# Kernel optimization log

Measured on AMD Instinct MI355X. Metric: run time of the kernel, lower is better.

The kernel has to match this reference:

```python
import jax, jax.numpy as jnp
import numpy as np
import math

B, S, D = 8, 1024, 1024
H, R = 16, 8
HD = D // H
SCALING = 16.0 / R  # alpha / rank = 2.0
DFF = 4 * D
DC = D // 2
NC = 3


def setup_inputs() -> dict:
    key = jax.random.key(0)
    ks = jax.random.split(key, 32)
    n = lambda i, shape, s=0.02: jax.random.normal(ks[i], shape, dtype=jnp.float32) * s
    inp = {
        'hidden_states': jax.random.normal(ks[0], (B, S, D), dtype=jnp.float32),
        # LoRA-adapted projections: base weight W [out,in], lora_A [r,in], lora_B [out,r]
        'Wq': n(1, (D, D)), 'Aq': n(2, (R, D), 0.1), 'Bq': n(3, (D, R), 0.02),
        'Wk': n(4, (D, D)), 'Ak': n(5, (R, D), 0.1), 'Bk': n(6, (D, R), 0.02),
        'Wv': n(7, (D, D)), 'Av': n(8, (R, D), 0.1), 'Bv': n(9, (D, R), 0.02),
        'Wo': n(10, (D, D)), 'Ao': n(11, (R, D), 0.1), 'Bo': n(12, (D, R), 0.02),
        'ln1_g': jnp.ones((D,), jnp.float32), 'ln1_b': jnp.zeros((D,), jnp.float32),
        'ln2_g': jnp.ones((D,), jnp.float32), 'ln2_b': jnp.zeros((D,), jnp.float32),
        'W1': n(13, (DFF, D)), 'b1': jnp.zeros((DFF,), jnp.float32),
        'W2': n(14, (D, DFF)), 'b2': jnp.zeros((D,), jnp.float32),
        'Wc1': n(15, (DC, D)), 'bc1': jnp.zeros((DC,), jnp.float32),
        'Wc2': n(16, (NC, DC)), 'bc2': jnp.zeros((NC,), jnp.float32),
    }
    return inp


def _lora_linear(x, W, A, Bm):
    # F.linear(x, W) + scaling * F.linear(F.linear(x, A), B)
    return x @ W.T + SCALING * ((x @ A.T) @ Bm.T)


def _layer_norm(x, g, b, eps=1e-5):
    mu = jnp.mean(x, axis=-1, keepdims=True)
    var = jnp.var(x, axis=-1, keepdims=True)
    return (x - mu) * jax.lax.rsqrt(var + eps) * g + b


def reference(hidden_states, Wq, Aq, Bq, Wk, Ak, Bk, Wv, Av, Bv, Wo, Ao, Bo,
              ln1_g, ln1_b, ln2_g, ln2_b, W1, b1, W2, b2, Wc1, bc1, Wc2, bc2):
    residual = hidden_states
    h = _layer_norm(hidden_states, ln1_g, ln1_b)
    # attention
    q = _lora_linear(h, Wq, Aq, Bq).reshape(B, S, H, HD).transpose(0, 2, 1, 3)
    k = _lora_linear(h, Wk, Ak, Bk).reshape(B, S, H, HD).transpose(0, 2, 1, 3)
    v = _lora_linear(h, Wv, Av, Bv).reshape(B, S, H, HD).transpose(0, 2, 1, 3)
    scores = jnp.einsum('bhqd,bhkd->bhqk', q, k) / math.sqrt(HD)
    probs = jax.nn.softmax(scores, axis=-1)
    ctx = jnp.einsum('bhqk,bhkd->bhqd', probs, v)
    ctx = ctx.transpose(0, 2, 1, 3).reshape(B, S, D)
    attn_out = _lora_linear(ctx, Wo, Ao, Bo)
    h = residual + attn_out
    residual = h
    hn = _layer_norm(h, ln2_g, ln2_b)
    ffn = jax.nn.gelu(hn @ W1.T + b1, approximate=False) @ W2.T + b2
    h = residual + ffn
    pooled = h[:, 0]  # [B, D]
    logits = jax.nn.gelu(pooled @ Wc1.T + bc1, approximate=False) @ Wc2.T + bc2
    return logits
```

## Files before the change

### kernel.cpp

```cpp
#include <hip/hip_runtime.h>
#include <hip/hip_bf16.h>


typedef __bf16 bf16x8 __attribute__((ext_vector_type(8)));
typedef float f32x4 __attribute__((ext_vector_type(4)));

__device__ __forceinline__ float bf2f(unsigned short u) {
  union { unsigned int i; float f; } v; v.i = ((unsigned int)u) << 16; return v.f;
}
__device__ __forceinline__ unsigned short f2bf(float f) {
  union { float f; unsigned int i; } v; v.f = f;
  unsigned int u = v.i;
  u += 0x7FFFu + ((u >> 16) & 1u);
  return (unsigned short)(u >> 16);
}
__device__ __forceinline__ float gelu_exact(float x) {
  return 0.5f * x * (1.0f + erff(x * 0.70710678118654752440f));
}

__global__ __launch_bounds__(256) void fold_kernel(
    const float* __restrict__ W, const float* __restrict__ A,
    const float* __restrict__ Bm, void* __restrict__ out, int out_bf16) {
  int i = blockIdx.x * 256 + threadIdx.x;
  int n = i >> 10, k = i & 1023;
  float acc = W[i];
#pragma unroll
  for (int r = 0; r < 8; ++r) acc += 2.0f * Bm[n * 8 + r] * A[r * 1024 + k];
  if (out_bf16) ((unsigned short*)out)[i] = f2bf(acc);
  else          ((float*)out)[i] = acc;
}

__global__ __launch_bounds__(256) void ln_kernel(
    const float* __restrict__ x, long in_stride, const float* __restrict__ g,
    const float* __restrict__ b, void* __restrict__ out, int out_bf16) {
  const float* xr = x + (size_t)blockIdx.x * in_stride;
  int t = threadIdx.x;
  float4 v = ((const float4*)xr)[t];
  float s  = v.x + v.y + v.z + v.w;
  float sq = v.x * v.x + v.y * v.y + v.z * v.z + v.w * v.w;
#pragma unroll
  for (int o = 32; o; o >>= 1) { s += __shfl_down(s, o); sq += __shfl_down(sq, o); }
  __shared__ float rs_[4], rq_[4], stat[2];
  int w = t >> 6, l = t & 63;
  if (l == 0) { rs_[w] = s; rq_[w] = sq; }
  __syncthreads();
  if (t == 0) {
    float S = rs_[0] + rs_[1] + rs_[2] + rs_[3];
    float Q = rq_[0] + rq_[1] + rq_[2] + rq_[3];
    float mu = S * (1.0f / 1024.0f);
    float var = Q * (1.0f / 1024.0f) - mu * mu;
    stat[0] = mu; stat[1] = rsqrtf(var + 1e-5f);
  }
  __syncthreads();
  float mu = stat[0], rstd = stat[1];
  float4 gg = ((const float4*)g)[t];
  float4 bb = ((const float4*)b)[t];
  float o0 = (v.x - mu) * rstd * gg.x + bb.x;
  float o1 = (v.y - mu) * rstd * gg.y + bb.y;
  float o2 = (v.z - mu) * rstd * gg.z + bb.z;
  float o3 = (v.w - mu) * rstd * gg.w + bb.w;
  if (out_bf16) {
    unsigned short* op = (unsigned short*)out + (size_t)blockIdx.x * 1024 + t * 4;
    op[0] = f2bf(o0); op[1] = f2bf(o1); op[2] = f2bf(o2); op[3] = f2bf(o3);
  } else {
    float* op = (float*)out + (size_t)blockIdx.x * 1024 + t * 4;
    op[0] = o0; op[1] = o1; op[2] = o2; op[3] = o3;
  }
}

__device__ __forceinline__ void gload_lds16(const void* g, void* l) {
  __builtin_amdgcn_global_load_lds(
      (__attribute__((address_space(1))) void*)(g),
      (__attribute__((address_space(3))) void*)(l), 16, 0, 0);
}

__global__ __launch_bounds__(256, 2) void gemm_kv(
    const unsigned short* __restrict__ h,
    const unsigned short* __restrict__ Wk, const unsigned short* __restrict__ Wv,
    unsigned short* __restrict__ Kout, unsigned short* __restrict__ Vout) {
  __shared__ unsigned short sA[128 * 32];
  __shared__ unsigned short sB[128 * 32];
  int wg = blockIdx.x;
  int swz = (wg & 7) * 128 + (wg >> 3);
  int proj = swz >> 9;
  int rem = swz & 511;
  int nb = rem & 7, mb = rem >> 3;
  const unsigned short* W = proj ? Wv : Wk;
  unsigned short* C = proj ? Vout : Kout;
  int brow = mb << 7, bcol = nb << 7;
  int t = threadIdx.x;
  int w = t >> 6, l = t & 63;
  int wr = (w >> 1) << 6, wc = (w & 1) << 6;
  int frow = l & 15, fk = (l >> 4) << 3;
  f32x4 acc[4][4];
#pragma unroll
  for (int m = 0; m < 4; ++m)
#pragma unroll
    for (int n = 0; n < 4; ++n) acc[m][n] = (f32x4){0.f, 0.f, 0.f, 0.f};
  int e0 = (w * 2) * 512 + l * 8;
  int e1 = e0 + 512;
  int r0 = e0 >> 5, c0 = e0 & 31;
  int r1 = e1 >> 5, c1 = e1 & 31;
  const unsigned short* gA0 = h + (size_t)(brow + r0) * 1024 + c0;
  const unsigned short* gA1 = h + (size_t)(brow + r1) * 1024 + c1;
  const unsigned short* gB0 = W + (size_t)(bcol + r0) * 1024 + c0;
  const unsigned short* gB1 = W + (size_t)(bcol + r1) * 1024 + c1;
  for (int kt = 0; kt < 1024; kt += 32) {
    gload_lds16(gA0 + kt, &sA[e0]);
    gload_lds16(gA1 + kt, &sA[e1]);
    gload_lds16(gB0 + kt, &sB[e0]);
    gload_lds16(gB1 + kt, &sB[e1]);
    __syncthreads();
    bf16x8 a[4], b[4];
#pragma unroll
    for (int m = 0; m < 4; ++m)
      a[m] = *(const bf16x8*)&sA[(wr + m * 16 + frow) * 32 + fk];
#pragma unroll
    for (int n = 0; n < 4; ++n)
      b[n] = *(const bf16x8*)&sB[(wc + n * 16 + frow) * 32 + fk];
#pragma unroll
    for (int m = 0; m < 4; ++m)
#pragma unroll
      for (int n = 0; n < 4; ++n)
        acc[m][n] = __builtin_amdgcn_mfma_f32_16x16x32_bf16(a[m], b[n], acc[m][n], 0, 0, 0);
    __syncthreads();
  }
  int crow = (l >> 4) << 2, ccol = l & 15;
#pragma unroll
  for (int m = 0; m < 4; ++m) {
    int gr = brow + wr + m * 16 + crow;
#pragma unroll
    for (int n = 0; n < 4; ++n) {
      int gc = bcol + wc + n * 16 + ccol;
#pragma unroll
      for (int j = 0; j < 4; ++j)
        C[(size_t)(gr + j) * 1024 + gc] = f2bf(acc[m][n][j]);
    }
  }
}

template <int CPW>
__global__ __launch_bounds__(256) void skinny_gemm(
    const float* __restrict__ X,
    const float* __restrict__ W,
    const float* __restrict__ bias,
    const float* __restrict__ resid, long rstride,
    float* __restrict__ Y, int N, int K, int do_gelu) {
  __shared__ float sX[8][1024];
  int t = threadIdx.x, w = t >> 6, l = t & 63;
  int col0 = blockIdx.x * (4 * CPW) + w * CPW;
  float acc[CPW][8];
#pragma unroll
  for (int c = 0; c < CPW; ++c)
#pragma unroll
    for (int m = 0; m < 8; ++m) acc[c][m] = 0.f;
  for (int kc = 0; kc < K; kc += 1024) {
    for (int i = t; i < 2048; i += 256) {
      int m = i >> 8, p = i & 255;
      ((float4*)sX[m])[p] = *(const float4*)(X + (size_t)m * K + kc + p * 4);
    }
    __syncthreads();
#pragma unroll
    for (int i = 0; i < 4; ++i) {
      int k = i * 256 + l * 4;
      float4 xv[8];
#pragma unroll
      for (int m = 0; m < 8; ++m) xv[m] = *(const float4*)&sX[m][k];
#pragma unroll
      for (int c = 0; c < CPW; ++c) {
        float4 wv = *(const float4*)(W + (size_t)(col0 + c) * K + kc + k);
#pragma unroll
        for (int m = 0; m < 8; ++m)
          acc[c][m] += wv.x * xv[m].x + wv.y * xv[m].y + wv.z * xv[m].z + wv.w * xv[m].w;
      }
    }
    __syncthreads();
  }
#pragma unroll
  for (int c = 0; c < CPW; ++c)
#pragma unroll
    for (int m = 0; m < 8; ++m) {
      float v = acc[c][m];
#pragma unroll
      for (int o = 32; o; o >>= 1) v += __shfl_down(v, o);
      acc[c][m] = v;
    }
  if (l == 0) {
#pragma unroll
    for (int c = 0; c < CPW; ++c) {
      int col = col0 + c;
      float bv = bias ? bias[col] : 0.f;
#pragma unroll
      for (int m = 0; m < 8; ++m) {
        float v = acc[c][m] + bv;
        if (do_gelu) v = gelu_exact(v);
        if (resid) v += resid[(size_t)m * rstride + col];
        Y[(size_t)m * N + col] = v;
      }
    }
  }
}

__global__ __launch_bounds__(256) void attn0_kernel(
    const float* __restrict__ q0, const unsigned short* __restrict__ K,
    const unsigned short* __restrict__ V, float* __restrict__ ctx) {
  int bh = blockIdx.x;
  int b = bh >> 4, hh = bh & 15;
  int t = threadIdx.x;
  __shared__ float sq[64];
  __shared__ float sp[1024];
  __shared__ float rbuf[8];
  __shared__ float sstat[2];
  __shared__ float part[4][64];
  if (t < 64) sq[t] = q0[b * 1024 + hh * 64 + t];
  __syncthreads();
  const unsigned short* Kb = K + (size_t)b * 1024 * 1024 + hh * 64;
  float sc[4], lmax = -1e30f;
#pragma unroll
  for (int i = 0; i < 4; ++i) {
    int k = t + i * 256;
    const unsigned short* Kr = Kb + (size_t)k * 1024;
    float s = 0.f;
#pragma unroll
    for (int d = 0; d < 64; d += 4) {
      ushort4 kv = *(const ushort4*)(Kr + d);
      s += sq[d] * bf2f(kv.x) + sq[d + 1] * bf2f(kv.y) +
           sq[d + 2] * bf2f(kv.z) + sq[d + 3] * bf2f(kv.w);
    }
    sc[i] = s * 0.125f;
    lmax = fmaxf(lmax, sc[i]);
  }
#pragma unroll
  for (int o = 32; o; o >>= 1) lmax = fmaxf(lmax, __shfl_down(lmax, o));
  int w = t >> 6, l = t & 63;
  if (l == 0) rbuf[w] = lmax;
  __syncthreads();
  if (t == 0) sstat[0] = fmaxf(fmaxf(rbuf[0], rbuf[1]), fmaxf(rbuf[2], rbuf[3]));
  __syncthreads();
  float gmax = sstat[0];
  float lsum = 0.f;
#pragma unroll
  for (int i = 0; i < 4; ++i) {
    float e = expf(sc[i] - gmax);
    sp[t + i * 256] = e;
    lsum += e;
  }
#pragma unroll
  for (int o = 32; o; o >>= 1) lsum += __shfl_down(lsum, o);
  if (l == 0) rbuf[4 + w] = lsum;
  __syncthreads();
  if (t == 0) sstat[1] = 1.0f / (rbuf[4] + rbuf[5] + rbuf[6] + rbuf[7]);
  __syncthreads();
  float inv = sstat[1];
  int d = t & 63, kq = t >> 6;
  const unsigned short* Vb = V + ((size_t)b * 1024 + kq * 256) * 1024 + hh * 64 + d;
  float a = 0.f;
  for (int k = 0; k < 256; ++k) a += sp[kq * 256 + k] * bf2f(Vb[(size_t)k * 1024]);
  part[kq][d] = a;
  __syncthreads();
  if (t < 64)
    ctx[b * 1024 + hh * 64 + t] =
        (part[0][t] + part[1][t] + part[2][t] + part[3][t]) * inv;
}

__global__ __launch_bounds__(256) void logits_kernel(
    const float* __restrict__ cmid, const float* __restrict__ Wc2,
    const float* __restrict__ bc2, float* __restrict__ out) {
  int t = threadIdx.x;
  int o = t >> 3, s = t & 7;
  float a = 0.f;
  if (o < 24) {
    int b = o / 3, n = o % 3;
    const float* x = cmid + b * 512 + s * 64;
    const float* w = Wc2 + n * 512 + s * 64;
#pragma unroll
    for (int k = 0; k < 64; ++k) a += x[k] * w[k];
  }
  __shared__ float part[32][8];
  part[o][s] = a;
  __syncthreads();
  if (t < 24) {
    float v = bc2[t % 3];
#pragma unroll
    for (int ss = 0; ss < 8; ++ss) v += part[t][ss];
    out[t] = v;
  }
}

extern "C" void kernel_launch(void* const* d_in, const int* in_sizes, int n_in,
                              void* d_out, int out_size, void* d_ws, size_t ws_size,
                              hipStream_t stream) {
  const float* x    = (const float*)d_in[0];
  const float* Wq   = (const float*)d_in[1];
  const float* Aq   = (const float*)d_in[2];
  const float* Bq   = (const float*)d_in[3];
  const float* Wk   = (const float*)d_in[4];
  const float* Ak   = (const float*)d_in[5];
  const float* Bk   = (const float*)d_in[6];
  const float* Wv   = (const float*)d_in[7];
  const float* Av   = (const float*)d_in[8];
  const float* Bv   = (const float*)d_in[9];
  const float* Wo   = (const float*)d_in[10];
  const float* Ao   = (const float*)d_in[11];
  const float* Bo   = (const float*)d_in[12];
  const float* ln1g = (const float*)d_in[13];
  const float* ln1b = (const float*)d_in[14];
  const float* ln2g = (const float*)d_in[15];
  const float* ln2b = (const float*)d_in[16];
  const float* W1   = (const float*)d_in[17];
  const float* b1   = (const float*)d_in[18];
  const float* W2   = (const float*)d_in[19];
  const float* b2   = (const float*)d_in[20];
  const float* Wc1  = (const float*)d_in[21];
  const float* bc1  = (const float*)d_in[22];
  const float* Wc2  = (const float*)d_in[23];
  const float* bc2  = (const float*)d_in[24];

  char* ws = (char*)d_ws;
  size_t off = 0;
  auto alloc = [&](size_t bytes) {
    void* p = ws + off;
    off += (bytes + 255) & ~(size_t)255;
    return p;
  };
  unsigned short* h_bf = (unsigned short*)alloc((size_t)8192 * 1024 * 2);
  unsigned short* WkE  = (unsigned short*)alloc((size_t)1024 * 1024 * 2);
  unsigned short* WvE  = (unsigned short*)alloc((size_t)1024 * 1024 * 2);
  float* WqE  = (float*)alloc((size_t)1024 * 1024 * 4);
  float* WoE  = (float*)alloc((size_t)1024 * 1024 * 4);
  unsigned short* Kb = (unsigned short*)alloc((size_t)8192 * 1024 * 2);
  unsigned short* Vb = (unsigned short*)alloc((size_t)8192 * 1024 * 2);
  float* x0   = (float*)alloc(8 * 1024 * 4);
  float* q0   = (float*)alloc(8 * 1024 * 4);
  float* ctx0 = (float*)alloc(8 * 1024 * 4);
  float* h2   = (float*)alloc(8 * 1024 * 4);
  float* hn   = (float*)alloc(8 * 1024 * 4);
  float* mid  = (float*)alloc(8 * 4096 * 4);
  float* pooled = (float*)alloc(8 * 1024 * 4);
  float* cmid = (float*)alloc(8 * 512 * 4);

  fold_kernel<<<4096, 256, 0, stream>>>(Wk, Ak, Bk, WkE, 1);
  fold_kernel<<<4096, 256, 0, stream>>>(Wv, Av, Bv, WvE, 1);
  fold_kernel<<<4096, 256, 0, stream>>>(Wq, Aq, Bq, WqE, 0);
  fold_kernel<<<4096, 256, 0, stream>>>(Wo, Ao, Bo, WoE, 0);
  ln_kernel<<<8192, 256, 0, stream>>>(x, 1024, ln1g, ln1b, h_bf, 1);
  ln_kernel<<<8, 256, 0, stream>>>(x, 1024 * 1024, ln1g, ln1b, x0, 0);
  gemm_kv<<<1024, 256, 0, stream>>>(h_bf, WkE, WvE, Kb, Vb);
  skinny_gemm<1><<<256, 256, 0, stream>>>(x0, WqE, nullptr, nullptr, 0,
                                          q0, 1024, 1024, 0);
  attn0_kernel<<<128, 256, 0, stream>>>(q0, Kb, Vb, ctx0);
  skinny_gemm<1><<<256, 256, 0, stream>>>(ctx0, WoE, nullptr, x, 1024 * 1024,
                                          h2, 1024, 1024, 0);
  ln_kernel<<<8, 256, 0, stream>>>(h2, 1024, ln2g, ln2b, hn, 0);
  skinny_gemm<4><<<256, 256, 0, stream>>>(hn, W1, b1, nullptr, 0,
                                          mid, 4096, 1024, 1);
  skinny_gemm<1><<<256, 256, 0, stream>>>(mid, W2, b2, h2, 1024,
                                          pooled, 1024, 4096, 0);
  skinny_gemm<1><<<128, 256, 0, stream>>>(pooled, Wc1, bc1, nullptr, 0,
                                          cmid, 512, 1024, 1);
  logits_kernel<<<1, 256, 0, stream>>>(cmid, Wc2, bc2, (float*)d_out);
}
```

Before: 156.4 us.

## Pull query back through K projection to skip full K/V GEMMs

Only token 0's output is needed, so K and V for all tokens are never materialised. The code instead computes qh = Wk_eff^T q per head, takes scores directly against the normalized hidden states, forms the probability-weighted sum of hidden states, and then applies the V projection once per head. LoRA weight folding is replaced by low-rank terms applied inside the skinny GEMM epilogue, and the two layernorm launches are merged into one. This removes the large bf16 MFMA GEMM and the weight-fold kernels, at the cost of streaming h_bf twice in memory-bound passes with fp32 scalar math.

```diff
diff --git a/kernel.cpp b/kernel.cpp
--- a/kernel.cpp
+++ b/kernel.cpp
@@ -2,11 +2,16 @@
 #include <hip/hip_bf16.h>
 
 
-typedef __bf16 bf16x8 __attribute__((ext_vector_type(8)));
 typedef float f32x4 __attribute__((ext_vector_type(4)));
 
 __device__ __forceinline__ float bf2f(unsigned short u) {
   union { unsigned int i; float f; } v; v.i = ((unsigned int)u) << 16; return v.f;
+}
+__device__ __forceinline__ float blo(unsigned int u) {
+  union { unsigned int i; float f; } v; v.i = u << 16; return v.f;
+}
+__device__ __forceinline__ float bhi(unsigned int u) {
+  union { unsigned int i; float f; } v; v.i = u & 0xffff0000u; return v.f;
 }
 __device__ __forceinline__ unsigned short f2bf(float f) {
   union { float f; unsigned int i; } v; v.f = f;
@@ -18,22 +23,14 @@
   return 0.5f * x * (1.0f + erff(x * 0.70710678118654752440f));
 }
 
-__global__ __launch_bounds__(256) void fold_kernel(
-    const float* __restrict__ W, const float* __restrict__ A,
-    const float* __restrict__ Bm, void* __restrict__ out, int out_bf16) {
-  int i = blockIdx.x * 256 + threadIdx.x;
-  int n = i >> 10, k = i & 1023;
-  float acc = W[i];
-#pragma unroll
-  for (int r = 0; r < 8; ++r) acc += 2.0f * Bm[n * 8 + r] * A[r * 1024 + k];
-  if (out_bf16) ((unsigned short*)out)[i] = f2bf(acc);
-  else          ((float*)out)[i] = acc;
-}
-
-__global__ __launch_bounds__(256) void ln_kernel(
-    const float* __restrict__ x, long in_stride, const float* __restrict__ g,
-    const float* __restrict__ b, void* __restrict__ out, int out_bf16) {
-  const float* xr = x + (size_t)blockIdx.x * in_stride;
+__global__ __launch_bounds__(256) void ln_fused(
+    const float* __restrict__ x, const float* __restrict__ g,
+    const float* __restrict__ b, unsigned short* __restrict__ hbf,
+    float* __restrict__ x0) {
+  int blk = blockIdx.x;
+  int f32out = (blk >= 8192);
+  const float* xr = f32out ? (x + (size_t)(blk - 8192) * 1048576)
+                           : (x + (size_t)blk * 1024);
   int t = threadIdx.x;
   float4 v = ((const float4*)xr)[t];
   float s  = v.x + v.y + v.z + v.w;
@@ -59,96 +56,62 @@
   float o1 = (v.y - mu) * rstd * gg.y + bb.y;
   float o2 = (v.z - mu) * rstd * gg.z + bb.z;
   float o3 = (v.w - mu) * rstd * gg.w + bb.w;
-  if (out_bf16) {
-    unsigned short* op = (unsigned short*)out + (size_t)blockIdx.x * 1024 + t * 4;
+  if (f32out) {
+    float* op = x0 + (size_t)(blk - 8192) * 1024 + t * 4;
+    op[0] = o0; op[1] = o1; op[2] = o2; op[3] = o3;
+  } else {
+    unsigned short* op = hbf + (size_t)blk * 1024 + t * 4;
     op[0] = f2bf(o0); op[1] = f2bf(o1); op[2] = f2bf(o2); op[3] = f2bf(o3);
-  } else {
-    float* op = (float*)out + (size_t)blockIdx.x * 1024 + t * 4;
-    op[0] = o0; op[1] = o1; op[2] = o2; op[3] = o3;
-  }
-}
-
-__device__ __forceinline__ void gload_lds16(const void* g, void* l) {
-  __builtin_amdgcn_global_load_lds(
-      (__attribute__((address_space(1))) void*)(g),
-      (__attribute__((address_space(3))) void*)(l), 16, 0, 0);
-}
-
-__global__ __launch_bounds__(256, 2) void gemm_kv(
-    const unsigned short* __restrict__ h,
-    const unsigned short* __restrict__ Wk, const unsigned short* __restrict__ Wv,
-    unsigned short* __restrict__ Kout, unsigned short* __restrict__ Vout) {
-  __shared__ unsigned short sA[128 * 32];
-  __shared__ unsigned short sB[128 * 32];
-  int wg = blockIdx.x;
-  int swz = (wg & 7) * 128 + (wg >> 3);
-  int proj = swz >> 9;
-  int rem = swz & 511;
-  int nb = rem & 7, mb = rem >> 3;
-  const unsigned short* W = proj ? Wv : Wk;
-  unsigned short* C = proj ? Vout : Kout;
-  int brow = mb << 7, bcol = nb << 7;
+  }
+}
+
+__global__ __launch_bounds__(256) void ln_kernel(
+    const float* __restrict__ x, long in_stride, const float* __restrict__ g,
+    const float* __restrict__ b, float* __restrict__ out) {
+  const float* xr = x + (size_t)blockIdx.x * in_stride;
   int t = threadIdx.x;
+  float4 v = ((const float4*)xr)[t];
+  float s  = v.x + v.y + v.z + v.w;
+  float sq = v.x * v.x + v.y * v.y + v.z * v.z + v.w * v.w;
+#pragma unroll
+  for (int o = 32; o; o >>= 1) { s += __shfl_down(s, o); sq += __shfl_down(sq, o); }
+  __shared__ float rs_[4], rq_[4], stat[2];
   int w = t >> 6, l = t & 63;
-  int wr = (w >> 1) << 6, wc = (w & 1) << 6;
-  int frow = l & 15, fk = (l >> 4) << 3;
-  f32x4 acc[4][4];
-#pragma unroll
-  for (int m = 0; m < 4; ++m)
-#pragma unroll
-    for (int n = 0; n < 4; ++n) acc[m][n] = (f32x4){0.f, 0.f, 0.f, 0.f};
-  int e0 = (w * 2) * 512 + l * 8;
-  int e1 = e0 + 512;
-  int r0 = e0 >> 5, c0 = e0 & 31;
-  int r1 = e1 >> 5, c1 = e1 & 31;
-  const unsigned short* gA0 = h + (size_t)(brow + r0) * 1024 + c0;
-  const unsigned short* gA1 = h + (size_t)(brow + r1) * 1024 + c1;
-  const unsigned short* gB0 = W + (size_t)(bcol + r0) * 1024 + c0;
-  const unsigned short* gB1 = W + (size_t)(bcol + r1) * 1024 + c1;
-  for (int kt = 0; kt < 1024; kt += 32) {
-    gload_lds16(gA0 + kt, &sA[e0]);
-    gload_lds16(gA1 + kt, &sA[e1]);
-    gload_lds16(gB0 + kt, &sB[e0]);
-    gload_lds16(gB1 + kt, &sB[e1]);
-    __syncthreads();
-    bf16x8 a[4], b[4];
-#pragma unroll
-    for (int m = 0; m < 4; ++m)
-      a[m] = *(const bf16x8*)&sA[(wr + m * 16 + frow) * 32 + fk];
-#pragma unroll
-    for (int n = 0; n < 4; ++n)
-      b[n] = *(const bf16x8*)&sB[(wc + n * 16 + frow) * 32 + fk];
-#pragma unroll
-    for (int m = 0; m < 4; ++m)
-#pragma unroll
-      for (int n = 0; n < 4; ++n)
-        acc[m][n] = __builtin_amdgcn_mfma_f32_16x16x32_bf16(a[m], b[n], acc[m][n], 0, 0, 0);
-    __syncthreads();
-  }
-  int crow = (l >> 4) << 2, ccol = l & 15;
-#pragma unroll
-  for (int m = 0; m < 4; ++m) {
-    int gr = brow + wr + m * 16 + crow;
-#pragma unroll
-    for (int n = 0; n < 4; ++n) {
-      int gc = bcol + wc + n * 16 + ccol;
-#pragma unroll
-      for (int j = 0; j < 4; ++j)
-        C[(size_t)(gr + j) * 1024 + gc] = f2bf(acc[m][n][j]);
-    }
-  }
+  if (l == 0) { rs_[w] = s; rq_[w] = sq; }
+  __syncthreads();
+  if (t == 0) {
+    float S = rs_[0] + rs_[1] + rs_[2] + rs_[3];
+    float Q = rq_[0] + rq_[1] + rq_[2] + rq_[3];
+    float mu = S * (1.0f / 1024.0f);
+    float var = Q * (1.0f / 1024.0f) - mu * mu;
+    stat[0] = mu; stat[1] = rsqrtf(var + 1e-5f);
+  }
+  __syncthreads();
+  float mu = stat[0], rstd = stat[1];
+  float4 gg = ((const float4*)g)[t];
+  float4 bb = ((const float4*)b)[t];
+  float* op = out + (size_t)blockIdx.x * 1024 + t * 4;
+  op[0] = (v.x - mu) * rstd * gg.x + bb.x;
+  op[1] = (v.y - mu) * rstd * gg.y + bb.y;
+  op[2] = (v.z - mu) * rstd * gg.z + bb.z;
+  op[3] = (v.w - mu) * rstd * gg.w + bb.w;
 }
 
 template <int CPW>
 __global__ __launch_bounds__(256) void skinny_gemm(
-    const float* __restrict__ X,
-    const float* __restrict__ W,
-    const float* __restrict__ bias,
+    const float* __restrict__ X, long xrs, long xhs,
+    const float* __restrict__ W, const float* __restrict__ bias,
+    const float* __restrict__ Amat, const float* __restrict__ Bmat,
     const float* __restrict__ resid, long rstride,
     float* __restrict__ Y, int N, int K, int do_gelu) {
   __shared__ float sX[8][1024];
+  __shared__ float sT[8][8][4];
+  __shared__ float T[8][8];
   int t = threadIdx.x, w = t >> 6, l = t & 63;
-  int col0 = blockIdx.x * (4 * CPW) + w * CPW;
+  int bcol = blockIdx.x * (4 * CPW);
+  int col0 = bcol + w * CPW;
+  int head = bcol >> 6;
+  const float* Xb = X + (size_t)head * xhs;
   float acc[CPW][8];
 #pragma unroll
   for (int c = 0; c < CPW; ++c)
@@ -157,9 +120,24 @@
   for (int kc = 0; kc < K; kc += 1024) {
     for (int i = t; i < 2048; i += 256) {
       int m = i >> 8, p = i & 255;
-      ((float4*)sX[m])[p] = *(const float4*)(X + (size_t)m * K + kc + p * 4);
+      ((float4*)sX[m])[p] = *(const float4*)(Xb + (size_t)m * xrs + kc + p * 4);
     }
     __syncthreads();
+    if (Amat && kc == 0) {
+      int m = t >> 5, r = (t >> 2) & 7, q = t & 3;
+      float s = 0.f;
+      const float* ar = Amat + r * 1024 + q * 256;
+      const float* xr = &sX[m][q * 256];
+      for (int j = 0; j < 256; j += 4)
+        s += xr[j] * ar[j] + xr[j+1] * ar[j+1] + xr[j+2] * ar[j+2] + xr[j+3] * ar[j+3];
+      sT[m][r][q] = s;
+      __syncthreads();
+      if (t < 64) {
+        int mm = t >> 3, rr = t & 7;
+        T[mm][rr] = sT[mm][rr][0] + sT[mm][rr][1] + sT[mm][rr][2] + sT[mm][rr][3];
+      }
+      __syncthreads();
+    }
 #pragma unroll
     for (int i = 0; i < 4; ++i) {
       int k = i * 256 + l * 4;
@@ -190,9 +168,18 @@
     for (int c = 0; c < CPW; ++c) {
       int col = col0 + c;
       float bv = bias ? bias[col] : 0.f;
+      float lb[8];
+      if (Amat) {
+#pragma unroll
+        for (int r = 0; r < 8; ++r) lb[r] = Bmat[col * 8 + r];
+      }
 #pragma unroll
       for (int m = 0; m < 8; ++m) {
         float v = acc[c][m] + bv;
+        if (Amat) {
+#pragma unroll
+          for (int r = 0; r < 8; ++r) v += 2.0f * lb[r] * T[m][r];
+        }
         if (do_gelu) v = gelu_exact(v);
         if (resid) v += resid[(size_t)m * rstride + col];
         Y[(size_t)m * N + col] = v;
@@ -201,66 +188,127 @@
   }
 }
 
-__global__ __launch_bounds__(256) void attn0_kernel(
-    const float* __restrict__ q0, const unsigned short* __restrict__ K,
-    const unsigned short* __restrict__ V, float* __restrict__ ctx) {
-  int bh = blockIdx.x;
-  int b = bh >> 4, hh = bh & 15;
+__global__ __launch_bounds__(256) void pullback_kernel(
+    const float* __restrict__ q0, const float* __restrict__ Wk,
+    const float* __restrict__ Ak, const float* __restrict__ Bk,
+    float* __restrict__ qh) {
+  int head = blockIdx.x >> 2, cchunk = blockIdx.x & 3;
   int t = threadIdx.x;
-  __shared__ float sq[64];
+  int c = cchunk * 256 + t;
+  __shared__ float sq[8][64];
+  __shared__ float sT[8][8][4];
+  __shared__ float T[8][8];
+  if (t < 512) { int b = t >> 6, d = t & 63; sq[b][d] = q0[b * 1024 + head * 64 + d]; }
+  __syncthreads();
+  {
+    int b = t >> 5, r = (t >> 2) & 7, q = t & 3;
+    float s = 0.f;
+#pragma unroll
+    for (int j = 0; j < 16; ++j) {
+      int d = q * 16 + j;
+      s += sq[b][d] * Bk[(head * 64 + d) * 8 + r];
+    }
+    sT[b][r][q] = s;
+  }
+  __syncthreads();
+  if (t < 64) {
+    int b = t >> 3, r = t & 7;
+    T[b][r] = sT[b][r][0] + sT[b][r][1] + sT[b][r][2] + sT[b][r][3];
+  }
+  __syncthreads();
+  float acc[8] = {0.f, 0.f, 0.f, 0.f, 0.f, 0.f, 0.f, 0.f};
+  for (int d = 0; d < 64; ++d) {
+    float wv = Wk[(size_t)(head * 64 + d) * 1024 + c];
+#pragma unroll
+    for (int b = 0; b < 8; ++b) acc[b] += sq[b][d] * wv;
+  }
+  float av[8];
+#pragma unroll
+  for (int r = 0; r < 8; ++r) av[r] = Ak[r * 1024 + c];
+#pragma unroll
+  for (int b = 0; b < 8; ++b) {
+    float v = acc[b];
+#pragma unroll
+    for (int r = 0; r < 8; ++r) v += 2.0f * T[b][r] * av[r];
+    qh[(size_t)(head * 8 + b) * 1024 + c] = v;
+  }
+}
+
+__global__ __launch_bounds__(256) void scores_kernel(
+    const float* __restrict__ qh, const unsigned short* __restrict__ hbf,
+    float* __restrict__ sraw) {
+  int blk = blockIdx.x;
+  int b = blk & 7, hh = (blk >> 3) & 15, khalf = blk >> 7;
+  int t = threadIdx.x, w = t >> 6, l = t & 63;
+  __shared__ float sq[1024];
+  for (int i = t; i < 1024; i += 256) sq[i] = qh[(size_t)(hh * 8 + b) * 1024 + i];
+  __syncthreads();
+  float qv[16];
+#pragma unroll
+  for (int j = 0; j < 16; ++j) qv[j] = sq[l * 16 + j];
+  const unsigned short* hb = hbf + (size_t)b * 1048576;
+  float* srow = sraw + (size_t)(hh * 8 + b) * 1024;
+  int kbase = khalf * 512 + w;
+  for (int i = 0; i < 128; ++i) {
+    int k = kbase + 4 * i;
+    const uint4* hp = (const uint4*)(hb + (size_t)k * 1024 + l * 16);
+    uint4 u0 = hp[0];
+    uint4 u1 = hp[1];
+    float s = qv[0] * blo(u0.x) + qv[1] * bhi(u0.x)
+            + qv[2] * blo(u0.y) + qv[3] * bhi(u0.y)
+            + qv[4] * blo(u0.z) + qv[5] * bhi(u0.z)
+            + qv[6] * blo(u0.w) + qv[7] * bhi(u0.w)
+            + qv[8] * blo(u1.x) + qv[9] * bhi(u1.x)
+            + qv[10] * blo(u1.y) + qv[11] * bhi(u1.y)
+            + qv[12] * blo(u1.z) + qv[13] * bhi(u1.z)
+            + qv[14] * blo(u1.w) + qv[15] * bhi(u1.w);
+#pragma unroll
+    for (int o = 1; o < 64; o <<= 1) s += __shfl_xor(s, o);
+    if (l == 0) srow[k] = s * 0.125f;
+  }
+}
+
+__global__ __launch_bounds__(256) void pv_kernel(
+    const float* __restrict__ sraw, const unsigned short* __restrict__ hbf,
+    float* __restrict__ pv) {
+  int blk = blockIdx.x;
+  int b = blk & 7, hh = (blk >> 3) & 15, chalf = blk >> 7;
+  int t = threadIdx.x, w = t >> 6, l = t & 63;
   __shared__ float sp[1024];
-  __shared__ float rbuf[8];
-  __shared__ float sstat[2];
-  __shared__ float part[4][64];
-  if (t < 64) sq[t] = q0[b * 1024 + hh * 64 + t];
-  __syncthreads();
-  const unsigned short* Kb = K + (size_t)b * 1024 * 1024 + hh * 64;
-  float sc[4], lmax = -1e30f;
-#pragma unroll
-  for (int i = 0; i < 4; ++i) {
-    int k = t + i * 256;
-    const unsigned short* Kr = Kb + (size_t)k * 1024;
-    float s = 0.f;
-#pragma unroll
-    for (int d = 0; d < 64; d += 4) {
-      ushort4 kv = *(const ushort4*)(Kr + d);
-      s += sq[d] * bf2f(kv.x) + sq[d + 1] * bf2f(kv.y) +
-           sq[d + 2] * bf2f(kv.z) + sq[d + 3] * bf2f(kv.w);
-    }
-    sc[i] = s * 0.125f;
-    lmax = fmaxf(lmax, sc[i]);
-  }
-#pragma unroll
-  for (int o = 32; o; o >>= 1) lmax = fmaxf(lmax, __shfl_down(lmax, o));
-  int w = t >> 6, l = t & 63;
-  if (l == 0) rbuf[w] = lmax;
-  __syncthreads();
-  if (t == 0) sstat[0] = fmaxf(fmaxf(rbuf[0], rbuf[1]), fmaxf(rbuf[2], rbuf[3]));
-  __syncthreads();
-  float gmax = sstat[0];
-  float lsum = 0.f;
-#pragma unroll
-  for (int i = 0; i < 4; ++i) {
-    float e = expf(sc[i] - gmax);
-    sp[t + i * 256] = e;
-    lsum += e;
-  }
+  __shared__ float red[8], stat[2];
+  const float* srow = sraw + (size_t)(hh * 8 + b) * 1024;
+  float4 s4 = ((const float4*)srow)[t];
+  float m4 = fmaxf(fmaxf(s4.x, s4.y), fmaxf(s4.z, s4.w));
+#pragma unroll
+  for (int o = 32; o; o >>= 1) m4 = fmaxf(m4, __shfl_down(m4, o));
+  if (l == 0) red[w] = m4;
+  __syncthreads();
+  if (t == 0) stat[0] = fmaxf(fmaxf(red[0], red[1]), fmaxf(red[2], red[3]));
+  __syncthreads();
+  float gmax = stat[0];
+  float e0 = expf(s4.x - gmax), e1 = expf(s4.y - gmax);
+  float e2 = expf(s4.z - gmax), e3 = expf(s4.w - gmax);
+  sp[t * 4] = e0; sp[t * 4 + 1] = e1; sp[t * 4 + 2] = e2; sp[t * 4 + 3] = e3;
+  float lsum = e0 + e1 + e2 + e3;
 #pragma unroll
   for (int o = 32; o; o >>= 1) lsum += __shfl_down(lsum, o);
-  if (l == 0) rbuf[4 + w] = lsum;
-  __syncthreads();
-  if (t == 0) sstat[1] = 1.0f / (rbuf[4] + rbuf[5] + rbuf[6] + rbuf[7]);
-  __syncthreads();
-  float inv = sstat[1];
-  int d = t & 63, kq = t >> 6;
-  const unsigned short* Vb = V + ((size_t)b * 1024 + kq * 256) * 1024 + hh * 64 + d;
-  float a = 0.f;
-  for (int k = 0; k < 256; ++k) a += sp[kq * 256 + k] * bf2f(Vb[(size_t)k * 1024]);
-  part[kq][d] = a;
-  __syncthreads();
-  if (t < 64)
-    ctx[b * 1024 + hh * 64 + t] =
-        (part[0][t] + part[1][t] + part[2][t] + part[3][t]) * inv;
+  if (l == 0) red[4 + w] = lsum;
+  __syncthreads();
+  if (t == 0) stat[1] = 1.0f / (red[4] + red[5] + red[6] + red[7]);
+  __syncthreads();
+  float inv = stat[1];
+  int c0 = chalf * 512 + t * 2;
+  const unsigned short* hp = hbf + (size_t)b * 1048576 + c0;
+  float a0 = 0.f, a1 = 0.f;
+  for (int k = 0; k < 1024; ++k) {
+    unsigned int u = *(const unsigned int*)(hp + (size_t)k * 1024);
+    float pk = sp[k];
+    a0 += pk * blo(u);
+    a1 += pk * bhi(u);
+  }
+  float* op = pv + (size_t)(hh * 8 + b) * 1024 + c0;
+  op[0] = a0 * inv;
+  op[1] = a1 * inv;
 }
 
 __global__ __launch_bounds__(256) void logits_kernel(
@@ -324,12 +372,9 @@
     return p;
   };
   unsigned short* h_bf = (unsigned short*)alloc((size_t)8192 * 1024 * 2);
-  unsigned short* WkE  = (unsigned short*)alloc((size_t)1024 * 1024 * 2);
-  unsigned short* WvE  = (unsigned short*)alloc((size_t)1024 * 1024 * 2);
-  float* WqE  = (float*)alloc((size_t)1024 * 1024 * 4);
-  float* WoE  = (float*)alloc((size_t)1024 * 1024 * 4);
-  unsigned short* Kb = (unsigned short*)alloc((size_t)8192 * 1024 * 2);
-  unsigned short* Vb = (unsigned short*)alloc((size_t)8192 * 1024 * 2);
+  float* qh   = (float*)alloc((size_t)128 * 1024 * 4);
+  float* sraw = (float*)alloc((size_t)128 * 1024 * 4);
+  float* pvb  = (float*)alloc((size_t)128 * 1024 * 4);
   float* x0   = (float*)alloc(8 * 1024 * 4);
   float* q0   = (float*)alloc(8 * 1024 * 4);
   float* ctx0 = (float*)alloc(8 * 1024 * 4);
@@ -339,24 +384,22 @@
   float* pooled = (float*)alloc(8 * 1024 * 4);
   float* cmid = (float*)alloc(8 * 512 * 4);
 
-  fold_kernel<<<4096, 256, 0, stream>>>(Wk, Ak, Bk, WkE, 1);
-  fold_kernel<<<4096, 256, 0, stream>>>(Wv, Av, Bv, WvE, 1);
-  fold_kernel<<<4096, 256, 0, stream>>>(Wq, Aq, Bq, WqE, 0);
-  fold_kernel<<<4096, 256, 0, stream>>>(Wo, Ao, Bo, WoE, 0);
-  ln_kernel<<<8192, 256, 0, stream>>>(x, 1024, ln1g, ln1b, h_bf, 1);
-  ln_kernel<<<8, 256, 0, stream>>>(x, 1024 * 1024, ln1g, ln1b, x0, 0);
-  gemm_kv<<<1024, 256, 0, stream>>>(h_bf, WkE, WvE, Kb, Vb);
-  skinny_gemm<1><<<256, 256, 0, stream>>>(x0, WqE, nullptr, nullptr, 0,
-                                          q0, 1024, 1024, 0);
-  attn0_kernel<<<128, 256, 0, stream>>>(q0, Kb, Vb, ctx0);
-  skinny_gemm<1><<<256, 256, 0, stream>>>(ctx0, WoE, nullptr, x, 1024 * 1024,
-                                          h2, 1024, 1024, 0);
-  ln_kernel<<<8, 256, 0, stream>>>(h2, 1024, ln2g, ln2b, hn, 0);
-  skinny_gemm<4><<<256, 256, 0, stream>>>(hn, W1, b1, nullptr, 0,
-                                          mid, 4096, 1024, 1);
-  skinny_gemm<1><<<256, 256, 0, stream>>>(mid, W2, b2, h2, 1024,
-                                          pooled, 1024, 4096, 0);
-  skinny_gemm<1><<<128, 256, 0, stream>>>(pooled, Wc1, bc1, nullptr, 0,
-                                          cmid, 512, 1024, 1);
+  ln_fused<<<8200, 256, 0, stream>>>(x, ln1g, ln1b, h_bf, x0);
+  skinny_gemm<1><<<256, 256, 0, stream>>>(x0, 1024, 0, Wq, nullptr, Aq, Bq,
+                                          nullptr, 0, q0, 1024, 1024, 0);
+  pullback_kernel<<<64, 256, 0, stream>>>(q0, Wk, Ak, Bk, qh);
+  scores_kernel<<<256, 256, 0, stream>>>(qh, h_bf, sraw);
+  pv_kernel<<<256, 256, 0, stream>>>(sraw, h_bf, pvb);
+  skinny_gemm<1><<<256, 256, 0, stream>>>(pvb, 1024, 8192, Wv, nullptr, Av, Bv,
+                                          nullptr, 0, ctx0, 1024, 1024, 0);
+  skinny_gemm<1><<<256, 256, 0, stream>>>(ctx0, 1024, 0, Wo, nullptr, Ao, Bo,
+                                          x, 1048576, h2, 1024, 1024, 0);
+  ln_kernel<<<8, 256, 0, stream>>>(h2, 1024, ln2g, ln2b, hn);
+  skinny_gemm<4><<<256, 256, 0, stream>>>(hn, 1024, 0, W1, b1, nullptr, nullptr,
+                                          nullptr, 0, mid, 4096, 1024, 1);
+  skinny_gemm<1><<<256, 256, 0, stream>>>(mid, 4096, 0, W2, b2, nullptr, nullptr,
+                                          h2, 1024, pooled, 1024, 4096, 0);
+  skinny_gemm<1><<<128, 256, 0, stream>>>(pooled, 1024, 0, Wc1, bc1, nullptr,
+                                          nullptr, nullptr, 0, cmid, 512, 1024, 1);
   logits_kernel<<<1, 256, 0, stream>>>(cmid, Wc2, bc2, (float*)d_out);
 }
```

Measured after the change: 221.1 us. +41.4%, slower.
